# Performance work log

Hardware: AMD Instinct MI355X
Metric: run time of the kernel (lower is better)

Reference implementation:

```python
import jax, jax.numpy as jnp
import numpy as np

N, D = 16384, 128

def setup_inputs() -> dict:
    key = jax.random.key(0)
    k1, k2 = jax.random.split(key)
    x = jax.random.normal(k1, (N, D), dtype=jnp.float32)
    adj = jax.random.randint(k2, (N, N), 0, 2, dtype=jnp.int32)
    return {"x": x, "adj": adj}

def reference(x, adj):
    # out[i] = x[i] + sum_{j: adj[i,j]==1} x[j]  ==  (adj + I) @ x
    a = adj.astype(x.dtype)
    return x + jnp.matmul(a, x)  # [N, D]
```

## Files before the change

kernel.cpp:

```cpp
#include <hip/hip_runtime.h>
#include <hip/hip_bf16.h>

#define GN 16384
#define GD 128

typedef __attribute__((ext_vector_type(8))) short short8;
typedef __attribute__((ext_vector_type(4))) float floatx4;
typedef __attribute__((ext_vector_type(4))) int intx4;

static __device__ __forceinline__ unsigned short f32_to_bf16(float f) {
  unsigned u = __builtin_bit_cast(unsigned, f);
  unsigned r = u + 0x7FFFu + ((u >> 16) & 1u);
  return (unsigned short)(r >> 16);
}

__global__ __launch_bounds__(256) void prep_kernel(const float* __restrict__ x,
                                                   float* __restrict__ out,
                                                   unsigned short* __restrict__ xT) {
  __shared__ unsigned short t[GD][66];
  const int tid = threadIdx.x;
  const int j0 = blockIdx.x * 64;
  for (int i = tid; i < 64 * GD; i += 256) {
    int j = i >> 7, d = i & (GD - 1);
    float v = x[(size_t)(j0 + j) * GD + d];
    out[(size_t)(j0 + j) * GD + d] = v;
    t[d][j] = f32_to_bf16(v);
  }
  __syncthreads();
  for (int i = tid; i < GD * 32; i += 256) {
    int d = i >> 5, jp = i & 31;
    unsigned lo = t[d][2 * jp], hi = t[d][2 * jp + 1];
    *reinterpret_cast<unsigned*>(xT + (size_t)d * GN + j0 + 2 * jp) = lo | (hi << 16);
  }
}

__global__ __launch_bounds__(256, 2) void gemm_kernel(const int* __restrict__ adj,
                                                      const unsigned short* __restrict__ xT,
                                                      float* __restrict__ out) {
  __shared__ unsigned short bbuf[2][32 * GD];
  const int tid = threadIdx.x;
  const int wave = tid >> 6;
  const int lane = tid & 63;
  const int q = lane >> 4;
  const int m = lane & 15;
  const int rbase = blockIdx.x * 128 + wave * 32;
  const int kbase = blockIdx.y * 4096;

  const int* arow0 = adj + (size_t)(rbase + m) * GN;
  const int* arow1 = adj + (size_t)(rbase + 16 + m) * GN;

  const int c1 = tid, c2 = tid + 256;
  const unsigned short* g1 = xT + (size_t)(c1 >> 2) * GN + (c1 & 3) * 8;
  const unsigned short* g2 = xT + (size_t)(c2 >> 2) * GN + (c2 & 3) * 8;
  unsigned short* l1 = &bbuf[0][0] + c1 * 8;
  unsigned short* l2 = &bbuf[0][0] + c2 * 8;

  floatx4 acc[2][8];
#pragma unroll
  for (int t = 0; t < 2; ++t)
#pragma unroll
    for (int c = 0; c < 8; ++c) acc[t][c] = (floatx4){0.f, 0.f, 0.f, 0.f};

#define STAGE_B(k0, buf)                                                               \
  do {                                                                                 \
    __builtin_amdgcn_global_load_lds(                                                  \
        (const __attribute__((address_space(1))) unsigned int*)(g1 + (k0)),            \
        (__attribute__((address_space(3))) unsigned int*)(l1 + (buf) * (32 * GD)),     \
        16, 0, 0);                                                                     \
    __builtin_amdgcn_global_load_lds(                                                  \
        (const __attribute__((address_space(1))) unsigned int*)(g2 + (k0)),            \
        (__attribute__((address_space(3))) unsigned int*)(l2 + (buf) * (32 * GD)),     \
        16, 0, 0);                                                                     \
  } while (0)

#define LOAD_ADJ(k0, r)                                                                \
  do {                                                                                 \
    const int kk_ = (k0) + q * 8;                                                      \
    r[0] = *(const intx4*)(arow0 + kk_);                                               \
    r[1] = *(const intx4*)(arow0 + kk_ + 4);                                           \
    r[2] = *(const intx4*)(arow1 + kk_);                                               \
    r[3] = *(const intx4*)(arow1 + kk_ + 4);                                           \
  } while (0)

  intx4 cur[4], nxt[4];
  STAGE_B(kbase, 0);
  LOAD_ADJ(kbase, cur);

  for (int i = 0; i < 128; ++i) {
    const int buf = i & 1;
    __syncthreads();

    const int knext = kbase + ((i + 1) & 127) * 32;
    STAGE_B(knext, buf ^ 1);
    LOAD_ADJ(knext, nxt);

    short8 bf[8];
    const unsigned short* bb = &bbuf[buf][0] + m * 32 + q * 8;
#pragma unroll
    for (int c = 0; c < 8; ++c) bf[c] = *(const short8*)(bb + c * 512);

    intx4 p0, p1;
    p0.x = (cur[0].x | (cur[0].y << 16)) * 0x3F80;
    p0.y = (cur[0].z | (cur[0].w << 16)) * 0x3F80;
    p0.z = (cur[1].x | (cur[1].y << 16)) * 0x3F80;
    p0.w = (cur[1].z | (cur[1].w << 16)) * 0x3F80;
    p1.x = (cur[2].x | (cur[2].y << 16)) * 0x3F80;
    p1.y = (cur[2].z | (cur[2].w << 16)) * 0x3F80;
    p1.z = (cur[3].x | (cur[3].y << 16)) * 0x3F80;
    p1.w = (cur[3].z | (cur[3].w << 16)) * 0x3F80;
    short8 af0 = __builtin_bit_cast(short8, p0);
    short8 af1 = __builtin_bit_cast(short8, p1);

#pragma unroll
    for (int c = 0; c < 8; ++c) {
      acc[0][c] = __builtin_amdgcn_mfma_f32_16x16x32_bf16(af0, bf[c], acc[0][c], 0, 0, 0);
      acc[1][c] = __builtin_amdgcn_mfma_f32_16x16x32_bf16(af1, bf[c], acc[1][c], 0, 0, 0);
    }

#pragma unroll
    for (int u = 0; u < 4; ++u) cur[u] = nxt[u];
  }

  const size_t obase = (size_t)rbase * GD;
#pragma unroll
  for (int t = 0; t < 2; ++t)
#pragma unroll
    for (int c = 0; c < 8; ++c)
#pragma unroll
      for (int r = 0; r < 4; ++r) {
        int row = t * 16 + q * 4 + r;
        int col = c * 16 + m;
        atomicAdd(out + obase + (size_t)row * GD + col, acc[t][c][r]);
      }
}

extern "C" void kernel_launch(void* const* d_in, const int* in_sizes, int n_in,
                              void* d_out, int out_size, void* d_ws, size_t ws_size,
                              hipStream_t stream) {
  const float* x = (const float*)d_in[0];
  const int* adj = (const int*)d_in[1];
  float* out = (float*)d_out;
  unsigned short* xT = (unsigned short*)d_ws;

  prep_kernel<<<GN / 64, 256, 0, stream>>>(x, out, xT);
  gemm_kernel<<<dim3(GN / 128, 4), 256, 0, stream>>>(adj, xT, out);
}
```

Before: 1.375 ms.

## Replace atomic split-K accumulation with partial buffers, larger swizzled B chunks, nontemporal adj loads

The GEMM now writes each K-split's partial result to its own workspace slab, and a new reduce kernel adds x plus the four partials, replacing float atomics on the output. The B-operand staging grows to 128-wide K chunks with an XOR swizzle in LDS to avoid bank conflicts, and sync points drop to one per four MFMA steps. The adjacency rows are read with nontemporal loads inside the loop instead of being register-prefetched one step ahead. The cost is an extra kernel launch, extra partial-buffer traffic, more LDS per block, and possibly exposed adj load latency.

```diff
diff --git a/kernel.cpp b/kernel.cpp
--- a/kernel.cpp
+++ b/kernel.cpp
@@ -3,6 +3,12 @@
 
 #define GN 16384
 #define GD 128
+#define KSPLIT 4
+#define KBLK (GN / KSPLIT)
+#define CHUNK_K 128
+#define NCHUNK (KBLK / CHUNK_K)
+#define CHUNK_SHORTS (GD * CHUNK_K)
+#define OUT_ELEMS (GN * GD)
 
 typedef __attribute__((ext_vector_type(8))) short short8;
 typedef __attribute__((ext_vector_type(4))) float floatx4;
@@ -15,16 +21,13 @@
 }
 
 __global__ __launch_bounds__(256) void prep_kernel(const float* __restrict__ x,
-                                                   float* __restrict__ out,
                                                    unsigned short* __restrict__ xT) {
   __shared__ unsigned short t[GD][66];
   const int tid = threadIdx.x;
   const int j0 = blockIdx.x * 64;
   for (int i = tid; i < 64 * GD; i += 256) {
     int j = i >> 7, d = i & (GD - 1);
-    float v = x[(size_t)(j0 + j) * GD + d];
-    out[(size_t)(j0 + j) * GD + d] = v;
-    t[d][j] = f32_to_bf16(v);
+    t[d][j] = f32_to_bf16(x[(size_t)(j0 + j) * GD + d]);
   }
   __syncthreads();
   for (int i = tid; i < GD * 32; i += 256) {
@@ -36,24 +39,40 @@
 
 __global__ __launch_bounds__(256, 2) void gemm_kernel(const int* __restrict__ adj,
                                                       const unsigned short* __restrict__ xT,
-                                                      float* __restrict__ out) {
-  __shared__ unsigned short bbuf[2][32 * GD];
+                                                      float* __restrict__ partials) {
+  __shared__ unsigned short bbuf[2][CHUNK_SHORTS];
   const int tid = threadIdx.x;
   const int wave = tid >> 6;
   const int lane = tid & 63;
   const int q = lane >> 4;
   const int m = lane & 15;
   const int rbase = blockIdx.x * 128 + wave * 32;
-  const int kbase = blockIdx.y * 4096;
+  const int kbase = blockIdx.y * KBLK;
 
-  const int* arow0 = adj + (size_t)(rbase + m) * GN;
-  const int* arow1 = adj + (size_t)(rbase + 16 + m) * GN;
+  const unsigned short* gptr[8];
+  unsigned short* lptr[8];
+#pragma unroll
+  for (int p = 0; p < 8; ++p) {
+    int s = tid + 256 * p;
+    int n = s >> 4;
+    int gsrc = (s & 15) ^ (n & 15);
+    gptr[p] = xT + (size_t)n * GN + kbase + gsrc * 8;
+    lptr[p] = &bbuf[0][0] + (size_t)s * 8;
+  }
 
-  const int c1 = tid, c2 = tid + 256;
-  const unsigned short* g1 = xT + (size_t)(c1 >> 2) * GN + (c1 & 3) * 8;
-  const unsigned short* g2 = xT + (size_t)(c2 >> 2) * GN + (c2 & 3) * 8;
-  unsigned short* l1 = &bbuf[0][0] + c1 * 8;
-  unsigned short* l2 = &bbuf[0][0] + c2 * 8;
+#define STAGE(bufsel, koff)                                                              \
+  do {                                                                                   \
+    _Pragma("unroll") for (int p = 0; p < 8; ++p) {                                      \
+      __builtin_amdgcn_global_load_lds(                                                  \
+          (const __attribute__((address_space(1))) unsigned int*)(gptr[p] + (koff)),     \
+          (__attribute__((address_space(3))) unsigned int*)(lptr[p] +                    \
+                                                           (bufsel) * CHUNK_SHORTS),     \
+          16, 0, 0);                                                                     \
+    }                                                                                    \
+  } while (0)
+
+  const int* a0 = adj + (size_t)(rbase + m) * GN + kbase + q * 8;
+  const int* a1 = adj + (size_t)(rbase + 16 + m) * GN + kbase + q * 8;
 
   floatx4 acc[2][8];
 #pragma unroll
@@ -61,77 +80,72 @@
 #pragma unroll
     for (int c = 0; c < 8; ++c) acc[t][c] = (floatx4){0.f, 0.f, 0.f, 0.f};
 
-#define STAGE_B(k0, buf)                                                               \
-  do {                                                                                 \
-    __builtin_amdgcn_global_load_lds(                                                  \
-        (const __attribute__((address_space(1))) unsigned int*)(g1 + (k0)),            \
-        (__attribute__((address_space(3))) unsigned int*)(l1 + (buf) * (32 * GD)),     \
-        16, 0, 0);                                                                     \
-    __builtin_amdgcn_global_load_lds(                                                  \
-        (const __attribute__((address_space(1))) unsigned int*)(g2 + (k0)),            \
-        (__attribute__((address_space(3))) unsigned int*)(l2 + (buf) * (32 * GD)),     \
-        16, 0, 0);                                                                     \
-  } while (0)
+  STAGE(0, 0);
 
-#define LOAD_ADJ(k0, r)                                                                \
-  do {                                                                                 \
-    const int kk_ = (k0) + q * 8;                                                      \
-    r[0] = *(const intx4*)(arow0 + kk_);                                               \
-    r[1] = *(const intx4*)(arow0 + kk_ + 4);                                           \
-    r[2] = *(const intx4*)(arow1 + kk_);                                               \
-    r[3] = *(const intx4*)(arow1 + kk_ + 4);                                           \
-  } while (0)
-
-  intx4 cur[4], nxt[4];
-  STAGE_B(kbase, 0);
-  LOAD_ADJ(kbase, cur);
-
-  for (int i = 0; i < 128; ++i) {
-    const int buf = i & 1;
+  int buf = 0;
+  for (int c = 0; c < NCHUNK; ++c) {
     __syncthreads();
-
-    const int knext = kbase + ((i + 1) & 127) * 32;
-    STAGE_B(knext, buf ^ 1);
-    LOAD_ADJ(knext, nxt);
-
-    short8 bf[8];
-    const unsigned short* bb = &bbuf[buf][0] + m * 32 + q * 8;
-#pragma unroll
-    for (int c = 0; c < 8; ++c) bf[c] = *(const short8*)(bb + c * 512);
-
-    intx4 p0, p1;
-    p0.x = (cur[0].x | (cur[0].y << 16)) * 0x3F80;
-    p0.y = (cur[0].z | (cur[0].w << 16)) * 0x3F80;
-    p0.z = (cur[1].x | (cur[1].y << 16)) * 0x3F80;
-    p0.w = (cur[1].z | (cur[1].w << 16)) * 0x3F80;
-    p1.x = (cur[2].x | (cur[2].y << 16)) * 0x3F80;
-    p1.y = (cur[2].z | (cur[2].w << 16)) * 0x3F80;
-    p1.z = (cur[3].x | (cur[3].y << 16)) * 0x3F80;
-    p1.w = (cur[3].z | (cur[3].w << 16)) * 0x3F80;
-    short8 af0 = __builtin_bit_cast(short8, p0);
-    short8 af1 = __builtin_bit_cast(short8, p1);
+    if (c < NCHUNK - 1) STAGE(buf ^ 1, (c + 1) * CHUNK_K);
 
 #pragma unroll
-    for (int c = 0; c < 8; ++c) {
-      acc[0][c] = __builtin_amdgcn_mfma_f32_16x16x32_bf16(af0, bf[c], acc[0][c], 0, 0, 0);
-      acc[1][c] = __builtin_amdgcn_mfma_f32_16x16x32_bf16(af1, bf[c], acc[1][c], 0, 0, 0);
-    }
+    for (int kk = 0; kk < 4; ++kk) {
+      const int koff = c * CHUNK_K + kk * 32;
+      intx4 r0 = __builtin_nontemporal_load((const intx4*)(a0 + koff));
+      intx4 r1 = __builtin_nontemporal_load((const intx4*)(a0 + koff + 4));
+      intx4 r2 = __builtin_nontemporal_load((const intx4*)(a1 + koff));
+      intx4 r3 = __builtin_nontemporal_load((const intx4*)(a1 + koff + 4));
+
+      short8 bf[8];
+      const unsigned short* bb = &bbuf[buf][0];
+      const int gsw = ((4 * kk + q) ^ m) * 8;
+#pragma unroll
+      for (int cc = 0; cc < 8; ++cc)
+        bf[cc] = *(const short8*)(bb + (cc * 16 + m) * CHUNK_K + gsw);
+
+      intx4 p0, p1;
+      p0.x = (r0.x | (r0.y << 16)) * 0x3F80;
+      p0.y = (r0.z | (r0.w << 16)) * 0x3F80;
+      p0.z = (r1.x | (r1.y << 16)) * 0x3F80;
+      p0.w = (r1.z | (r1.w << 16)) * 0x3F80;
+      p1.x = (r2.x | (r2.y << 16)) * 0x3F80;
+      p1.y = (r2.z | (r2.w << 16)) * 0x3F80;
+      p1.z = (r3.x | (r3.y << 16)) * 0x3F80;
+      p1.w = (r3.z | (r3.w << 16)) * 0x3F80;
+      short8 af0 = __builtin_bit_cast(short8, p0);
+      short8 af1 = __builtin_bit_cast(short8, p1);
 
 #pragma unroll
-    for (int u = 0; u < 4; ++u) cur[u] = nxt[u];
+      for (int cc = 0; cc < 8; ++cc) {
+        acc[0][cc] = __builtin_amdgcn_mfma_f32_16x16x32_bf16(af0, bf[cc], acc[0][cc], 0, 0, 0);
+        acc[1][cc] = __builtin_amdgcn_mfma_f32_16x16x32_bf16(af1, bf[cc], acc[1][cc], 0, 0, 0);
+      }
+    }
+    buf ^= 1;
   }
 
-  const size_t obase = (size_t)rbase * GD;
+  float* pp = partials + (size_t)blockIdx.y * OUT_ELEMS + (size_t)rbase * GD;
 #pragma unroll
   for (int t = 0; t < 2; ++t)
 #pragma unroll
-    for (int c = 0; c < 8; ++c)
+    for (int cc = 0; cc < 8; ++cc)
 #pragma unroll
       for (int r = 0; r < 4; ++r) {
         int row = t * 16 + q * 4 + r;
-        int col = c * 16 + m;
-        atomicAdd(out + obase + (size_t)row * GD + col, acc[t][c][r]);
+        int col = cc * 16 + m;
+        pp[(size_t)row * GD + col] = acc[t][cc][r];
       }
+}
+
+__global__ __launch_bounds__(256) void reduce_kernel(const float* __restrict__ x,
+                                                     const float* __restrict__ partials,
+                                                     float* __restrict__ out) {
+  size_t i = ((size_t)blockIdx.x * 256 + threadIdx.x) * 4;
+  floatx4 v = *(const floatx4*)(x + i);
+  v += *(const floatx4*)(partials + 0 * (size_t)OUT_ELEMS + i);
+  v += *(const floatx4*)(partials + 1 * (size_t)OUT_ELEMS + i);
+  v += *(const floatx4*)(partials + 2 * (size_t)OUT_ELEMS + i);
+  v += *(const floatx4*)(partials + 3 * (size_t)OUT_ELEMS + i);
+  *(floatx4*)(out + i) = v;
 }
 
 extern "C" void kernel_launch(void* const* d_in, const int* in_sizes, int n_in,
@@ -141,7 +155,9 @@
   const int* adj = (const int*)d_in[1];
   float* out = (float*)d_out;
   unsigned short* xT = (unsigned short*)d_ws;
+  float* partials = (float*)((char*)d_ws + (size_t)GN * GD * 2);
 
-  prep_kernel<<<GN / 64, 256, 0, stream>>>(x, out, xT);
-  gemm_kernel<<<dim3(GN / 128, 4), 256, 0, stream>>>(adj, xT, out);
+  prep_kernel<<<GN / 64, 256, 0, stream>>>(x, xT);
+  gemm_kernel<<<dim3(GN / 128, KSPLIT), 256, 0, stream>>>(adj, xT, partials);
+  reduce_kernel<<<OUT_ELEMS / 4 / 256, 256, 0, stream>>>(x, partials, out);
 }
```

After: 1.428 ms. +3.9%, slower.
